# Optimization experiments

Measured on AMD Instinct MI355X. Metric: run time of the kernel, lower is better.

## Reference

```python
import jax, jax.numpy as jnp
import numpy as np

# ---- static config (from module __init__ defaults) ----
INPUT_DIM = 3
NUM_LEVELS = 16
LEVEL_DIM = 2
SCALE = 2.0
BASE_RES = 16
LOG2_T = 19
MAX_T = 2 ** LOG2_T
NUM_FREQS = 6
N_POINTS = 2_000_000
PRIMES = np.array([1, 2654435761, 805459861], dtype=np.uint32)  # Instant-NGP spatial hash primes
CORNERS = np.array([[i, j, k] for i in (0, 1) for j in (0, 1) for k in (0, 1)], dtype=np.int32)  # [8,3]

RES = [int(np.floor(BASE_RES * SCALE ** l)) for l in range(NUM_LEVELS)]
SIZES = [min(MAX_T, (r + 1) ** 3) for r in RES]  # dense if the full grid fits in the hashmap
OFFSETS = np.concatenate([[0], np.cumsum(SIZES)]).astype(np.int64)
TOTAL = int(OFFSETS[-1])  # 7,131,219 rows


def setup_inputs() -> dict:
    key = jax.random.key(0)
    k1, k2 = jax.random.split(key)
    x = jax.random.uniform(k1, (N_POINTS, INPUT_DIM), dtype=jnp.float32)  # points in [0,1]^3
    # hash-grid features init U(-1e-4, 1e-4) as in Instant-NGP
    table = (jax.random.uniform(k2, (TOTAL, LEVEL_DIM), dtype=jnp.float32) * 2.0 - 1.0) * 1e-4
    return {"x": x, "table": table}


def _level_interp(x, table_l, res, size):
    """Trilinear hash-grid interpolation at one level. x:[N,3] in [0,1]."""
    pos = x * jnp.float32(res)            # [N,3]
    p0f = jnp.floor(pos)
    frac = pos - p0f                      # [N,3]
    p0 = p0f.astype(jnp.int32)
    corners = jnp.clip(p0[:, None, :] + CORNERS[None], 0, res)  # [N,8,3], grid has res+1 verts
    if (res + 1) ** 3 <= MAX_T:
        # dense stride indexing
        r1 = res + 1
        idx = corners[..., 0] + corners[..., 1] * r1 + corners[..., 2] * (r1 * r1)
    else:
        c = corners.astype(jnp.uint32)
        h = (c[..., 0] * jnp.uint32(int(PRIMES[0]))
             ^ c[..., 1] * jnp.uint32(int(PRIMES[1]))
             ^ c[..., 2] * jnp.uint32(int(PRIMES[2])))
        idx = (h % jnp.uint32(size)).astype(jnp.int32)
    vals = table_l[idx]                   # [N,8,level_dim] gather
    # trilinear weights: prod over dims of (frac if corner==1 else 1-frac)
    w = jnp.where(CORNERS[None] == 1, frac[:, None, :], 1.0 - frac[:, None, :]).prod(-1)  # [N,8]
    return jnp.einsum('nc,ncd->nd', w, vals)  # [N,level_dim]


def _hash_encode(x, table):
    feats = [
        _level_interp(x, table[int(OFFSETS[l]):int(OFFSETS[l + 1])], RES[l], SIZES[l])
        for l in range(NUM_LEVELS)
    ]
    return jnp.concatenate(feats, axis=-1)  # [N, num_levels*level_dim]


def _pos_encode(x):
    coeffs = jnp.float32(2.0) ** jnp.arange(NUM_FREQS, dtype=jnp.float32)  # log_sampling
    xc = x[:, None, :] * coeffs[None, :, None]           # [N,F,3]
    sc = jnp.stack([jnp.sin(xc), jnp.cos(xc)], axis=2)   # [N,F,2,3] -> order: per-freq sin(3) then cos(3)
    return jnp.concatenate([x, sc.reshape(x.shape[0], 2 * NUM_FREQS * INPUT_DIM)], axis=-1)


def reference(x, table):
    hash_feat = _hash_encode(x, table)   # [N,32]
    freq_feat = _pos_encode(x)           # [N,39]
    return jnp.concatenate([hash_feat, freq_feat], axis=-1)  # [N,71]
```

## Files before the change

### kernel.cpp

```cpp
#include <hip/hip_runtime.h>

typedef float f4 __attribute__((ext_vector_type(4)));

#define BLK 128
#define NLEV 16
#define NHASH 13

__constant__ int kOff[NLEV] = {0, 4913, 40850, 315475, 839763, 1364051, 1888339,
                               2412627, 2936915, 3461203, 3985491, 4509779,
                               5034067, 5558355, 6082643, 6606931};

__global__ __launch_bounds__(256)
void levels_kernel(const float* __restrict__ xs, const float2* __restrict__ tab,
                   unsigned* __restrict__ scratch, int n)
{
    const int lev = blockIdx.y;
    const int i   = blockIdx.x * 256 + threadIdx.x;
    if (i >= n) return;

    const int res = 16 << (3 + lev);
    const float2* __restrict__ tl = tab + kOff[3 + lev];

    const float px = __builtin_nontemporal_load(&xs[3 * i + 0]);
    const float py = __builtin_nontemporal_load(&xs[3 * i + 1]);
    const float pz = __builtin_nontemporal_load(&xs[3 * i + 2]);

    const float fres = (float)res;
    float posx = px * fres, posy = py * fres, posz = pz * fres;
    float fxf = floorf(posx), fyf = floorf(posy), fzf = floorf(posz);
    float rx = posx - fxf, ry = posy - fyf, rz = posz - fzf;

    const unsigned mask = 524287u;
    unsigned hx  = (unsigned)(int)fxf;
    unsigned hy0 = (unsigned)(int)fyf * 2654435761u;
    unsigned hy1 = hy0 + 2654435761u;
    unsigned hz0 = (unsigned)(int)fzf * 805459861u;
    unsigned hz1 = hz0 + 805459861u;
    unsigned h00 = hy0 ^ hz0, h01 = hy0 ^ hz1, h10 = hy1 ^ hz0, h11 = hy1 ^ hz1;

    float2 v000, v001, v010, v011, v100, v101, v110, v111;
    if ((hx & 1u) == 0u) {
        #define PAIRH(H, VA, VB) { \
            unsigned ia = (hx ^ (H)) & mask; \
            f4 q = *(const f4*)(tl + (ia & ~1u)); \
            bool sw = (ia & 1u) != 0u; \
            VA.x = sw ? q.z : q.x; VA.y = sw ? q.w : q.y; \
            VB.x = sw ? q.x : q.z; VB.y = sw ? q.y : q.w; }
        PAIRH(h00, v000, v100)
        PAIRH(h01, v001, v101)
        PAIRH(h10, v010, v110)
        PAIRH(h11, v011, v111)
        #undef PAIRH
    } else {
        unsigned hx1 = hx + 1u;
        v000 = tl[(hx ^ h00) & mask]; v100 = tl[(hx1 ^ h00) & mask];
        v001 = tl[(hx ^ h01) & mask]; v101 = tl[(hx1 ^ h01) & mask];
        v010 = tl[(hx ^ h10) & mask]; v110 = tl[(hx1 ^ h10) & mask];
        v011 = tl[(hx ^ h11) & mask]; v111 = tl[(hx1 ^ h11) & mask];
    }

    float wx1 = rx, wx0 = 1.f - rx;
    float wy1 = ry, wy0 = 1.f - ry;
    float wz1 = rz, wz0 = 1.f - rz;

    float f0, f1, w;
    w = wx0 * wy0 * wz0; f0  = w * v000.x; f1  = w * v000.y;
    w = wx0 * wy0 * wz1; f0 += w * v001.x; f1 += w * v001.y;
    w = wx0 * wy1 * wz0; f0 += w * v010.x; f1 += w * v010.y;
    w = wx0 * wy1 * wz1; f0 += w * v011.x; f1 += w * v011.y;
    w = wx1 * wy0 * wz0; f0 += w * v100.x; f1 += w * v100.y;
    w = wx1 * wy0 * wz1; f0 += w * v101.x; f1 += w * v101.y;
    w = wx1 * wy1 * wz0; f0 += w * v110.x; f1 += w * v110.y;
    w = wx1 * wy1 * wz1; f0 += w * v111.x; f1 += w * v111.y;

    unsigned packed = (__float_as_uint(f0) >> 16) | (__float_as_uint(f1) & 0xFFFF0000u);
    __builtin_nontemporal_store(packed, &scratch[(size_t)lev * n + i]);
}

__global__ __launch_bounds__(BLK)
void final_kernel(const float* __restrict__ xs, const float* __restrict__ table,
                  const unsigned* __restrict__ scratch, float* __restrict__ out, int n)
{
    __shared__ float sbuf[BLK * 71];
    const int tid  = threadIdx.x;
    const int base = blockIdx.x * BLK;
    const int pi   = base + tid;

    float px = 0.f, py = 0.f, pz = 0.f;
    if (pi < n) {
        px = xs[3 * pi + 0];
        py = xs[3 * pi + 1];
        pz = xs[3 * pi + 2];
    }

    float* srow = sbuf + tid * 71;
    const float2* __restrict__ tab = (const float2*)table;

    #pragma unroll
    for (int l = 0; l < 3; ++l) {
        const int res = 16 << l;
        const float2* __restrict__ tl = tab + kOff[l];
        const float fres = (float)res;

        float posx = px * fres, posy = py * fres, posz = pz * fres;
        float fxf = floorf(posx), fyf = floorf(posy), fzf = floorf(posz);
        float rx = posx - fxf, ry = posy - fyf, rz = posz - fzf;

        const unsigned r1 = (unsigned)(res + 1);
        const unsigned r2 = r1 * r1;
        unsigned x0 = (unsigned)(int)fxf;
        unsigned by0 = (unsigned)(int)fyf * r1; unsigned by1 = by0 + r1;
        unsigned cz0 = (unsigned)(int)fzf * r2; unsigned cz1 = cz0 + r2;

        float2 v000, v001, v010, v011, v100, v101, v110, v111;
        #define PAIRD(B, VA, VB) { \
            unsigned i0 = x0 + (B); \
            if ((i0 & 1u) == 0u) { f4 q = *(const f4*)(tl + i0); \
                VA.x = q.x; VA.y = q.y; VB.x = q.z; VB.y = q.w; } \
            else { VA = tl[i0]; VB = tl[i0 + 1u]; } }
        PAIRD(by0 + cz0, v000, v100)
        PAIRD(by0 + cz1, v001, v101)
        PAIRD(by1 + cz0, v010, v110)
        PAIRD(by1 + cz1, v011, v111)
        #undef PAIRD

        float wx1 = rx, wx0 = 1.f - rx;
        float wy1 = ry, wy0 = 1.f - ry;
        float wz1 = rz, wz0 = 1.f - rz;

        float f0, f1, w;
        w = wx0 * wy0 * wz0; f0  = w * v000.x; f1  = w * v000.y;
        w = wx0 * wy0 * wz1; f0 += w * v001.x; f1 += w * v001.y;
        w = wx0 * wy1 * wz0; f0 += w * v010.x; f1 += w * v010.y;
        w = wx0 * wy1 * wz1; f0 += w * v011.x; f1 += w * v011.y;
        w = wx1 * wy0 * wz0; f0 += w * v100.x; f1 += w * v100.y;
        w = wx1 * wy0 * wz1; f0 += w * v101.x; f1 += w * v101.y;
        w = wx1 * wy1 * wz0; f0 += w * v110.x; f1 += w * v110.y;
        w = wx1 * wy1 * wz1; f0 += w * v111.x; f1 += w * v111.y;

        srow[2 * l]     = f0;
        srow[2 * l + 1] = f1;
    }

    if (pi < n) {
        #pragma unroll
        for (int h = 0; h < NHASH; ++h) {
            unsigned u = __builtin_nontemporal_load(&scratch[(size_t)h * n + pi]);
            srow[6 + 2 * h] = __uint_as_float(u << 16);
            srow[7 + 2 * h] = __uint_as_float(u & 0xFFFF0000u);
        }
    }

    srow[32] = px; srow[33] = py; srow[34] = pz;
    float coef = 1.f;
    #pragma unroll
    for (int f = 0; f < 6; ++f) {
        float s, c;
        __sincosf(px * coef, &s, &c); srow[35 + 6*f + 0] = s; srow[35 + 6*f + 3] = c;
        __sincosf(py * coef, &s, &c); srow[35 + 6*f + 1] = s; srow[35 + 6*f + 4] = c;
        __sincosf(pz * coef, &s, &c); srow[35 + 6*f + 2] = s; srow[35 + 6*f + 5] = c;
        coef *= 2.f;
    }

    __syncthreads();

    const int nvalid = min(BLK, n - base);
    float* obase = out + (size_t)base * 71;
    if (nvalid == BLK) {
        f4* o4 = (f4*)obase;
        const f4* s4 = (const f4*)sbuf;
        #pragma unroll 1
        for (int i = tid; i < (BLK * 71) / 4; i += BLK)
            __builtin_nontemporal_store(s4[i], &o4[i]);
    } else {
        #pragma unroll 1
        for (int i = tid; i < nvalid * 71; i += BLK)
            __builtin_nontemporal_store(sbuf[i], &obase[i]);
    }
}

extern "C" void kernel_launch(void* const* d_in, const int* in_sizes, int n_in,
                              void* d_out, int out_size, void* d_ws, size_t ws_size,
                              hipStream_t stream) {
    const float* xs    = (const float*)d_in[0];
    const float* table = (const float*)d_in[1];
    float* out = (float*)d_out;
    const int n = in_sizes[0] / 3;

    unsigned* scratch = (unsigned*)d_ws;
    const float2* tab = (const float2*)table;

    const int bpl = (n + 255) / 256;
    hipLaunchKernelGGL(levels_kernel, dim3(bpl, NHASH), dim3(256), 0, stream,
                       xs, tab, scratch, n);

    const int gf = (n + BLK - 1) / BLK;
    hipLaunchKernelGGL(final_kernel, dim3(gf), dim3(BLK), 0, stream,
                       xs, table, scratch, out, n);
}
```

Measured before the change: 881.4 us.

## Convert hash-level tables to packed bf16 and process two points per thread

Adds a pre-pass that truncates the 13 hashed level tables to packed bf16 pairs (4 bytes per entry) in workspace, halving the bytes fetched per random gather and making each level's table 2 MB so it fits better in cache. The levels kernel now handles two points per thread, issuing all paired loads first for more memory-level parallelism, and factors the trilinear weights. The table is truncated to bf16 before interpolation rather than only the output, which adds rounding error. An extra conversion pass over about 27 MB of table runs on every call. A float32 fallback is kept for when the workspace is too small.

```diff
diff --git a/kernel.cpp b/kernel.cpp
--- a/kernel.cpp
+++ b/kernel.cpp
@@ -5,19 +5,107 @@
 #define BLK 128
 #define NLEV 16
 #define NHASH 13
+#define HSIZE 524288
+#define HMASK 524287u
+#define KOFF3 315475
 
 __constant__ int kOff[NLEV] = {0, 4913, 40850, 315475, 839763, 1364051, 1888339,
                                2412627, 2936915, 3461203, 3985491, 4509779,
                                5034067, 5558355, 6082643, 6606931};
 
 __global__ __launch_bounds__(256)
-void levels_kernel(const float* __restrict__ xs, const float2* __restrict__ tab,
+void convert_kernel(const float2* __restrict__ tab, unsigned* __restrict__ tbf)
+{
+    const int i = blockIdx.x * 256 + threadIdx.x;
+    if (i >= NHASH * HSIZE) return;
+    float2 v = tab[KOFF3 + i];
+    tbf[i] = (__float_as_uint(v.x) >> 16) | (__float_as_uint(v.y) & 0xFFFF0000u);
+}
+
+__global__ __launch_bounds__(256)
+void levels_kernel(const float* __restrict__ xs, const unsigned* __restrict__ tbf,
                    unsigned* __restrict__ scratch, int n)
+{
+    const int lev = blockIdx.y;
+    const int i0  = blockIdx.x * 512 + threadIdx.x;
+    const int res = 16 << (3 + lev);
+    const float fres = (float)res;
+    const unsigned* __restrict__ tl = tbf + (size_t)lev * HSIZE;
+
+    unsigned hx[2], hc[2][4];
+    float rx[2], ry[2], rz[2];
+    bool valid[2];
+
+    #pragma unroll
+    for (int p = 0; p < 2; ++p) {
+        const int i = i0 + p * 256;
+        valid[p] = (i < n);
+        float px = 0.f, py = 0.f, pz = 0.f;
+        if (valid[p]) {
+            px = __builtin_nontemporal_load(&xs[3 * i + 0]);
+            py = __builtin_nontemporal_load(&xs[3 * i + 1]);
+            pz = __builtin_nontemporal_load(&xs[3 * i + 2]);
+        }
+        float posx = px * fres, posy = py * fres, posz = pz * fres;
+        float fxf = floorf(posx), fyf = floorf(posy), fzf = floorf(posz);
+        rx[p] = posx - fxf; ry[p] = posy - fyf; rz[p] = posz - fzf;
+        unsigned x  = (unsigned)(int)fxf;
+        unsigned y0 = (unsigned)(int)fyf * 2654435761u, y1 = y0 + 2654435761u;
+        unsigned z0 = (unsigned)(int)fzf * 805459861u,  z1 = z0 + 805459861u;
+        hx[p] = x;
+        hc[p][0] = y0 ^ z0; hc[p][1] = y0 ^ z1; hc[p][2] = y1 ^ z0; hc[p][3] = y1 ^ z1;
+    }
+
+    unsigned va[2][4], vb[2][4];
+    #pragma unroll
+    for (int p = 0; p < 2; ++p) {
+        #pragma unroll
+        for (int c = 0; c < 4; ++c) {
+            unsigned ia = (hx[p] ^ hc[p][c]) & HMASK;
+            uint2 q = *(const uint2*)(tl + (ia & ~1u));
+            va[p][c] = (ia & 1u) ? q.y : q.x;
+            vb[p][c] = (ia & 1u) ? q.x : q.y;
+        }
+    }
+    #pragma unroll
+    for (int p = 0; p < 2; ++p) {
+        if (hx[p] & 1u) {
+            unsigned x1 = hx[p] + 1u;
+            #pragma unroll
+            for (int c = 0; c < 4; ++c)
+                vb[p][c] = tl[(x1 ^ hc[p][c]) & HMASK];
+        }
+    }
+
+    #pragma unroll
+    for (int p = 0; p < 2; ++p) {
+        if (!valid[p]) continue;
+        float wx1 = rx[p], wx0 = 1.f - wx1;
+        float wy1 = ry[p], wy0 = 1.f - wy1;
+        float wz1 = rz[p], wz0 = 1.f - wz1;
+        float wc[4] = {wy0 * wz0, wy0 * wz1, wy1 * wz0, wy1 * wz1};
+        float f0 = 0.f, f1 = 0.f;
+        #pragma unroll
+        for (int c = 0; c < 4; ++c) {
+            float a0 = __uint_as_float(va[p][c] << 16);
+            float a1 = __uint_as_float(va[p][c] & 0xFFFF0000u);
+            float b0 = __uint_as_float(vb[p][c] << 16);
+            float b1 = __uint_as_float(vb[p][c] & 0xFFFF0000u);
+            f0 += wc[c] * (wx0 * a0 + wx1 * b0);
+            f1 += wc[c] * (wx0 * a1 + wx1 * b1);
+        }
+        unsigned packed = (__float_as_uint(f0) >> 16) | (__float_as_uint(f1) & 0xFFFF0000u);
+        __builtin_nontemporal_store(packed, &scratch[(size_t)lev * n + (i0 + p * 256)]);
+    }
+}
+
+__global__ __launch_bounds__(256)
+void levels_f32_kernel(const float* __restrict__ xs, const float2* __restrict__ tab,
+                       unsigned* __restrict__ scratch, int n)
 {
     const int lev = blockIdx.y;
     const int i   = blockIdx.x * 256 + threadIdx.x;
     if (i >= n) return;
-
     const int res = 16 << (3 + lev);
     const float2* __restrict__ tl = tab + kOff[3 + lev];
 
@@ -30,34 +118,16 @@
     float fxf = floorf(posx), fyf = floorf(posy), fzf = floorf(posz);
     float rx = posx - fxf, ry = posy - fyf, rz = posz - fzf;
 
-    const unsigned mask = 524287u;
     unsigned hx  = (unsigned)(int)fxf;
-    unsigned hy0 = (unsigned)(int)fyf * 2654435761u;
-    unsigned hy1 = hy0 + 2654435761u;
-    unsigned hz0 = (unsigned)(int)fzf * 805459861u;
-    unsigned hz1 = hz0 + 805459861u;
+    unsigned hy0 = (unsigned)(int)fyf * 2654435761u, hy1 = hy0 + 2654435761u;
+    unsigned hz0 = (unsigned)(int)fzf * 805459861u,  hz1 = hz0 + 805459861u;
     unsigned h00 = hy0 ^ hz0, h01 = hy0 ^ hz1, h10 = hy1 ^ hz0, h11 = hy1 ^ hz1;
 
-    float2 v000, v001, v010, v011, v100, v101, v110, v111;
-    if ((hx & 1u) == 0u) {
-        #define PAIRH(H, VA, VB) { \
-            unsigned ia = (hx ^ (H)) & mask; \
-            f4 q = *(const f4*)(tl + (ia & ~1u)); \
-            bool sw = (ia & 1u) != 0u; \
-            VA.x = sw ? q.z : q.x; VA.y = sw ? q.w : q.y; \
-            VB.x = sw ? q.x : q.z; VB.y = sw ? q.y : q.w; }
-        PAIRH(h00, v000, v100)
-        PAIRH(h01, v001, v101)
-        PAIRH(h10, v010, v110)
-        PAIRH(h11, v011, v111)
-        #undef PAIRH
-    } else {
-        unsigned hx1 = hx + 1u;
-        v000 = tl[(hx ^ h00) & mask]; v100 = tl[(hx1 ^ h00) & mask];
-        v001 = tl[(hx ^ h01) & mask]; v101 = tl[(hx1 ^ h01) & mask];
-        v010 = tl[(hx ^ h10) & mask]; v110 = tl[(hx1 ^ h10) & mask];
-        v011 = tl[(hx ^ h11) & mask]; v111 = tl[(hx1 ^ h11) & mask];
-    }
+    unsigned hx1 = hx + 1u;
+    float2 v000 = tl[(hx ^ h00) & HMASK], v100 = tl[(hx1 ^ h00) & HMASK];
+    float2 v001 = tl[(hx ^ h01) & HMASK], v101 = tl[(hx1 ^ h01) & HMASK];
+    float2 v010 = tl[(hx ^ h10) & HMASK], v110 = tl[(hx1 ^ h10) & HMASK];
+    float2 v011 = tl[(hx ^ h11) & HMASK], v111 = tl[(hx1 ^ h11) & HMASK];
 
     float wx1 = rx, wx0 = 1.f - rx;
     float wy1 = ry, wy0 = 1.f - ry;
@@ -188,11 +258,22 @@
     const int n = in_sizes[0] / 3;
 
     unsigned* scratch = (unsigned*)d_ws;
+    const size_t featBytes = (size_t)NHASH * (size_t)n * 4u;
+    const size_t needBf16  = featBytes + (size_t)NHASH * HSIZE * 4u;
     const float2* tab = (const float2*)table;
 
-    const int bpl = (n + 255) / 256;
-    hipLaunchKernelGGL(levels_kernel, dim3(bpl, NHASH), dim3(256), 0, stream,
-                       xs, tab, scratch, n);
+    if (ws_size >= needBf16) {
+        unsigned* tbf = (unsigned*)((char*)d_ws + featBytes);
+        const int gc = (NHASH * HSIZE + 255) / 256;
+        hipLaunchKernelGGL(convert_kernel, dim3(gc), dim3(256), 0, stream, tab, tbf);
+        const int bpl = (n + 511) / 512;
+        hipLaunchKernelGGL(levels_kernel, dim3(bpl, NHASH), dim3(256), 0, stream,
+                           xs, tbf, scratch, n);
+    } else {
+        const int bpl = (n + 255) / 256;
+        hipLaunchKernelGGL(levels_f32_kernel, dim3(bpl, NHASH), dim3(256), 0, stream,
+                           xs, tab, scratch, n);
+    }
 
     const int gf = (n + BLK - 1) / BLK;
     hipLaunchKernelGGL(final_kernel, dim3(gf), dim3(BLK), 0, stream,
```

New measurement: 892.6 us. About the same (+1.3%).
